# Kernel tuning notes

Measured on AMD Instinct MI355X. Metric: run time of the kernel, lower is better.

Reference implementation:

```python
import jax, jax.numpy as jnp
import numpy as np

N = 50000      # nodes
E = 800000     # edges (avg degree 16)
D_IN = 128     # node_feature_dim
H = 256        # hidden_dim
EPS = 1e-5     # BatchNorm eps


def setup_inputs() -> dict:
    key = jax.random.key(0)
    ks = jax.random.split(key, 32)
    inp = {
        "x": jax.random.normal(ks[0], (N, D_IN), jnp.float32),
        "edge_index": jax.random.randint(ks[1], (2, E), 0, N, jnp.int32),
    }
    dims = [(D_IN, H), (H, H), (H, H)]
    k = 2
    for i, (din, dout) in enumerate(dims):
        s = 1.0 / np.sqrt(din)
        inp[f"Wl{i}"] = jax.random.uniform(ks[k], (din, dout), jnp.float32, -s, s); k += 1
        inp[f"bl{i}"] = jax.random.uniform(ks[k], (dout,), jnp.float32, -s, s); k += 1
        inp[f"Wr{i}"] = jax.random.uniform(ks[k], (din, dout), jnp.float32, -s, s); k += 1
        inp[f"g{i}"] = jnp.ones((dout,), jnp.float32)
        inp[f"b{i}"] = jnp.zeros((dout,), jnp.float32)
        inp[f"rm{i}"] = jax.random.normal(ks[k], (dout,), jnp.float32) * 0.1; k += 1
        inp[f"rv{i}"] = jax.random.uniform(ks[k], (dout,), jnp.float32, 0.5, 1.5); k += 1
    return inp


def _sage(x, src, dst, Wl, bl, Wr):
    # PyG SAGEConv (aggr='mean'): out = lin_l(mean_{j in N(i)} x_j) + lin_r(x_i)
    deg = jax.ops.segment_sum(jnp.ones((src.shape[0],), x.dtype), dst, num_segments=N)
    agg = jax.ops.segment_sum(x[src], dst, num_segments=N)  # [N, d_in]
    mean = agg / jnp.maximum(deg, 1.0)[:, None]
    return mean @ Wl + bl + x @ Wr


def _bn(x, g, b, rm, rv):
    # eval-mode BatchNorm1d with running stats
    return (x - rm) * (g * jax.lax.rsqrt(rv + EPS)) + b


def reference(x, edge_index,
              Wl0, bl0, Wr0, g0, b0, rm0, rv0,
              Wl1, bl1, Wr1, g1, b1, rm1, rv1,
              Wl2, bl2, Wr2, g2, b2, rm2, rv2):
    src, dst = edge_index[0], edge_index[1]
    h = jax.nn.relu(_bn(_sage(x, src, dst, Wl0, bl0, Wr0), g0, b0, rm0, rv0))
    h = jax.nn.relu(_bn(_sage(h, src, dst, Wl1, bl1, Wr1), g1, b1, rm1, rv1))
    h = _bn(_sage(h, src, dst, Wl2, bl2, Wr2), g2, b2, rm2, rv2)
    return h  # [N, H] node embeddings (dropout is identity in eval mode)
```

## Files before the change

kernel.cpp:

```cpp
#include <hip/hip_runtime.h>
#include <hip/hip_bf16.h>

#define NNODES 50000
#define NEDGES 800000
#define HID 256
#define BN_EPS 1e-5f
#define SCAN_B ((NNODES + 255) / 256)

typedef __attribute__((ext_vector_type(8))) short short8v;
typedef __attribute__((ext_vector_type(4))) float f32x4;
typedef __attribute__((ext_vector_type(2))) float f32x2;

__device__ inline void load_lds16(const void* g, void* l) {
    __builtin_amdgcn_global_load_lds(
        (const __attribute__((address_space(1))) unsigned int*)g,
        (__attribute__((address_space(3))) unsigned int*)l, 16, 0, 0);
}

__global__ void k_countrank(const int* __restrict__ ei, int* __restrict__ cnt,
                            int* __restrict__ rank, int nE) {
    int e = blockIdx.x * blockDim.x + threadIdx.x;
    if (e < nE) rank[e] = atomicAdd(&cnt[ei[nE + e]], 1);
}

__global__ void k_bsum(const int* __restrict__ cnt, int* __restrict__ loc,
                       int* __restrict__ bsum, int n) {
    __shared__ int sh[256];
    int tid = threadIdx.x;
    int i = blockIdx.x * 256 + tid;
    int v = (i < n) ? cnt[i] : 0;
    sh[tid] = v;
    __syncthreads();
    for (int off = 1; off < 256; off <<= 1) {
        int t = (tid >= off) ? sh[tid - off] : 0;
        __syncthreads();
        sh[tid] += t;
        __syncthreads();
    }
    if (i < n) loc[i] = sh[tid] - v;
    if (tid == 255) bsum[blockIdx.x] = sh[255];
}

__global__ void k_bscan(int* __restrict__ bsum, int nb) {
    __shared__ int sh[256];
    int tid = threadIdx.x;
    int v = (tid < nb) ? bsum[tid] : 0;
    sh[tid] = v;
    __syncthreads();
    for (int off = 1; off < 256; off <<= 1) {
        int t = (tid >= off) ? sh[tid - off] : 0;
        __syncthreads();
        sh[tid] += t;
        __syncthreads();
    }
    if (tid < nb) bsum[tid] = sh[tid] - v;
}

__global__ void k_addoff(const int* __restrict__ loc, const int* __restrict__ bsum,
                         int* __restrict__ rowptr, int n, int nE) {
    int i = blockIdx.x * 256 + threadIdx.x;
    if (i < n) rowptr[i] = loc[i] + bsum[blockIdx.x];
    if (i == 0) rowptr[n] = nE;
}

__global__ void k_fill2(const int* __restrict__ ei, const int* __restrict__ rowptr,
                        const int* __restrict__ rank, int* __restrict__ col, int nE) {
    int e = blockIdx.x * blockDim.x + threadIdx.x;
    if (e < nE) col[rowptr[ei[nE + e]] + rank[e]] = ei[e];
}

#define PREP_CAST 1600000
#define PREP_TR   327680
__global__ void k_prep(const float* __restrict__ x,
                       __hip_bfloat16* __restrict__ xb, unsigned char* __restrict__ x8,
                       const float* __restrict__ s0, const float* __restrict__ s1,
                       const float* __restrict__ s2, const float* __restrict__ s3,
                       const float* __restrict__ s4, const float* __restrict__ s5,
                       __hip_bfloat16* __restrict__ d0, __hip_bfloat16* __restrict__ d1,
                       __hip_bfloat16* __restrict__ d2, __hip_bfloat16* __restrict__ d3,
                       __hip_bfloat16* __restrict__ d4, __hip_bfloat16* __restrict__ d5,
                       int* __restrict__ cnt) {
    int f = blockIdx.x * blockDim.x + threadIdx.x;
    if (f < PREP_CAST) {
        float4 v = *(const float4*)(x + f * 4);
        union { uint2 u; unsigned short s[4]; } ob;
        ob.s[0] = __bfloat16_as_ushort(__float2bfloat16(v.x));
        ob.s[1] = __bfloat16_as_ushort(__float2bfloat16(v.y));
        ob.s[2] = __bfloat16_as_ushort(__float2bfloat16(v.z));
        ob.s[3] = __bfloat16_as_ushort(__float2bfloat16(v.w));
        *(uint2*)(xb + f * 4) = ob.u;
        int p = __builtin_amdgcn_cvt_pk_fp8_f32(v.x, v.y, 0, false);
        p = __builtin_amdgcn_cvt_pk_fp8_f32(v.z, v.w, p, true);
        *(int*)(x8 + f * 4) = p;
    } else if (f < PREP_CAST + PREP_TR) {
        int r = f - PREP_CAST;
        const float* src; __hip_bfloat16* dst; int K; int i;
        if (r < 65536) {
            K = 128;
            if (r < 32768) { src = s0; dst = d0; i = r; }
            else           { src = s1; dst = d1; i = r - 32768; }
        } else {
            K = 256;
            int q = r - 65536;
            int wsel = q >> 16;
            i = q & 65535;
            src = (wsel == 0) ? s2 : (wsel == 1) ? s3 : (wsel == 2) ? s4 : s5;
            dst = (wsel == 0) ? d2 : (wsel == 1) ? d3 : (wsel == 2) ? d4 : d5;
        }
        int k = i >> 8;
        int nn = i & 255;
        dst[nn * K + k] = __float2bfloat16(src[i]);
    } else {
        int i = f - PREP_CAST - PREP_TR;
        if (i < NNODES) cnt[i] = 0;
    }
}

template <int D, int U>
__global__ void k_meanf8(const unsigned char* __restrict__ x8,
                         const int* __restrict__ rowptr, const int* __restrict__ col,
                         __hip_bfloat16* __restrict__ mean, int n) {
    constexpr int CPL = D / 16;
    constexpr int R = 64 / CPL;
    int gw = (blockIdx.x * blockDim.x + threadIdx.x) >> 6;
    int lane = threadIdx.x & 63;
    if (gw >= n) return;
    int beg = rowptr[gw], end = rowptr[gw + 1];
    int sub = lane / CPL;
    int fpos = lane % CPL;
    const uint4* base = (const uint4*)x8;

    float acc[16];
#pragma unroll
    for (int j = 0; j < 16; j++) acc[j] = 0.f;

    for (int p0 = beg; p0 < end; p0 += U * R) {
        int idx[U]; bool ok[U];
#pragma unroll
        for (int u = 0; u < U; u++) {
            int p = p0 + u * R + sub;
            ok[u] = (p < end);
            idx[u] = ok[u] ? col[p] : 0;
        }
        uint4 v[U];
#pragma unroll
        for (int u = 0; u < U; u++) {
            uint4 t = {0u, 0u, 0u, 0u};
            if (ok[u]) t = base[(size_t)idx[u] * CPL + fpos];
            v[u] = t;
        }
#pragma unroll
        for (int u = 0; u < U; u++) {
            const unsigned int uu[4] = {v[u].x, v[u].y, v[u].z, v[u].w};
#pragma unroll
            for (int q = 0; q < 4; q++) {
                f32x2 lo = __builtin_amdgcn_cvt_pk_f32_fp8(uu[q], false);
                f32x2 hi = __builtin_amdgcn_cvt_pk_f32_fp8(uu[q], true);
                acc[4 * q + 0] += lo.x;
                acc[4 * q + 1] += lo.y;
                acc[4 * q + 2] += hi.x;
                acc[4 * q + 3] += hi.y;
            }
        }
    }

    if constexpr (R >= 8) {
#pragma unroll
        for (int j = 0; j < 16; j++) acc[j] += __shfl_xor(acc[j], 8, 64);
    }
#pragma unroll
    for (int j = 0; j < 16; j++) acc[j] += __shfl_xor(acc[j], 16, 64);
#pragma unroll
    for (int j = 0; j < 16; j++) acc[j] += __shfl_xor(acc[j], 32, 64);

    if (sub == 0) {
        float inv = (end > beg) ? 1.f / (float)(end - beg) : 0.f;
        union { uint4 v[2]; unsigned short s[16]; } o;
#pragma unroll
        for (int j = 0; j < 16; j++)
            o.s[j] = __bfloat16_as_ushort(__float2bfloat16(acc[j] * inv));
        uint4* dst = (uint4*)(mean + (size_t)gw * D + fpos * 16);
        dst[0] = o.v[0];
        dst[1] = o.v[1];
    }
}

template <int KH, typename OutT, int RELU, int W8>
__launch_bounds__(256, 2)
__global__ void k_gemm3(const __hip_bfloat16* __restrict__ A1,
                        const __hip_bfloat16* __restrict__ A2,
                        const __hip_bfloat16* __restrict__ W1t,
                        const __hip_bfloat16* __restrict__ W2t,
                        const float* __restrict__ bl,
                        const float* __restrict__ g,
                        const float* __restrict__ bb,
                        const float* __restrict__ rm,
                        const float* __restrict__ rv,
                        OutT* __restrict__ out, unsigned char* __restrict__ out8,
                        int n) {
    constexpr int NSTEP = KH / 16;
    constexpr int K8TOT = KH / 4;
    __shared__ uint4 ldsv[4096];
    char* lds = (char*)ldsv;
    int tid = threadIdx.x;
    int l = (blockIdx.x & 7) * (gridDim.x >> 3) + (blockIdx.x >> 3);
    int rb = l >> 2, ct = l & 3;
    int colbase = ct * 64;

#pragma unroll
    for (int it = 0; it < K8TOT / 4; it++) {
        int j = tid + it * 256;
        int k8 = j >> 6, c = j & 63;
        const __hip_bfloat16* src =
            (k8 < KH / 8) ? (W1t + (size_t)(colbase + c) * KH + k8 * 8)
                          : (W2t + (size_t)(colbase + c) * KH + (k8 - KH / 8) * 8);
        load_lds16(src, lds + (size_t)j * 16);
    }

    int lane = tid & 63, wv = tid >> 6;
    int quad = lane >> 4, ml = lane & 15;
    int row0 = rb * 256 + wv * 64;

    const short8v* p1[4];
    const short8v* p2[4];
#pragma unroll
    for (int i = 0; i < 4; i++) {
        int r = row0 + i * 16 + ml;
        if (r > n - 1) r = n - 1;
        p1[i] = (const short8v*)(A1 + (size_t)r * KH) + quad;
        p2[i] = (const short8v*)(A2 + (size_t)r * KH) + quad;
    }

    f32x4 acc[4][4];
#pragma unroll
    for (int i = 0; i < 4; i++)
#pragma unroll
        for (int t = 0; t < 4; t++) acc[i][t] = {0.f, 0.f, 0.f, 0.f};

    short8v ab[4][4];
#pragma unroll
    for (int s = 0; s < 3; s++) {
        const short8v* const* pp = (s < NSTEP / 2) ? p1 : p2;
        int sh = (s < NSTEP / 2) ? s : s - NSTEP / 2;
#pragma unroll
        for (int i = 0; i < 4; i++) ab[s][i] = pp[i][sh * 4];
    }
    __syncthreads();

#pragma unroll
    for (int s = 0; s < NSTEP; s++) {
        int sn = s + 3;
        if (sn < NSTEP) {
            const short8v* const* pp = (sn < NSTEP / 2) ? p1 : p2;
            int sh = (sn < NSTEP / 2) ? sn : sn - NSTEP / 2;
#pragma unroll
            for (int i = 0; i < 4; i++) ab[sn & 3][i] = pp[i][sh * 4];
        }
        short8v bfr[4];
#pragma unroll
        for (int t = 0; t < 4; t++)
            bfr[t] = *(const short8v*)(lds + ((size_t)((s * 4 + quad) * 64 + t * 16 + ml)) * 16);
#pragma unroll
        for (int t = 0; t < 4; t++)
#pragma unroll
            for (int i = 0; i < 4; i++)
                acc[i][t] = __builtin_amdgcn_mfma_f32_16x16x32_bf16(
                    ab[s & 3][i], bfr[t], acc[i][t], 0, 0, 0);
    }

    __syncthreads();
    float* scr = (float*)(lds + wv * 16384);
#pragma unroll
    for (int t = 0; t < 4; t++) {
        int c = colbase + t * 16 + ml;
        float sv = g[c] * rsqrtf(rv[c] + BN_EPS);
        float tv = (bl[c] - rm[c]) * sv + bb[c];
#pragma unroll
        for (int i = 0; i < 4; i++)
#pragma unroll
            for (int r = 0; r < 4; r++) {
                float v = acc[i][t][r] * sv + tv;
                if (RELU) v = fmaxf(v, 0.f);
                scr[(i * 16 + quad * 4 + r) * 64 + t * 16 + ml] = v;
            }
    }
    int rl8 = lane >> 3, c8 = (lane & 7) * 8;
#pragma unroll
    for (int p = 0; p < 8; p++) {
        int rowl = p * 8 + rl8;
        int row = row0 + rowl;
        f32x4 v0 = *(const f32x4*)(scr + rowl * 64 + c8);
        f32x4 v1 = *(const f32x4*)(scr + rowl * 64 + c8 + 4);
        if (row < n) {
            if constexpr (sizeof(OutT) == 2) {
                union { uint4 u; unsigned short s[8]; } o;
                o.s[0] = __bfloat16_as_ushort(__float2bfloat16(v0.x));
                o.s[1] = __bfloat16_as_ushort(__float2bfloat16(v0.y));
                o.s[2] = __bfloat16_as_ushort(__float2bfloat16(v0.z));
                o.s[3] = __bfloat16_as_ushort(__float2bfloat16(v0.w));
                o.s[4] = __bfloat16_as_ushort(__float2bfloat16(v1.x));
                o.s[5] = __bfloat16_as_ushort(__float2bfloat16(v1.y));
                o.s[6] = __bfloat16_as_ushort(__float2bfloat16(v1.z));
                o.s[7] = __bfloat16_as_ushort(__float2bfloat16(v1.w));
                *(uint4*)(out + (size_t)row * HID + colbase + c8) = o.u;
            } else {
                float* dst = (float*)out + (size_t)row * HID + colbase + c8;
                *(f32x4*)dst = v0;
                *(f32x4*)(dst + 4) = v1;
            }
            if constexpr (W8) {
                int lo = __builtin_amdgcn_cvt_pk_fp8_f32(v0.x, v0.y, 0, false);
                lo = __builtin_amdgcn_cvt_pk_fp8_f32(v0.z, v0.w, lo, true);
                int hi = __builtin_amdgcn_cvt_pk_fp8_f32(v1.x, v1.y, 0, false);
                hi = __builtin_amdgcn_cvt_pk_fp8_f32(v1.z, v1.w, hi, true);
                uint2 u2 = {(unsigned)lo, (unsigned)hi};
                *(uint2*)(out8 + (size_t)row * HID + colbase + c8) = u2;
            }
        }
    }
}

extern "C" void kernel_launch(void* const* d_in, const int* in_sizes, int n_in,
                              void* d_out, int out_size, void* d_ws, size_t ws_size,
                              hipStream_t stream) {
    const float* x = (const float*)d_in[0];
    const int* ei = (const int*)d_in[1];
    const float *Wl[3], *blv[3], *Wr[3], *g[3], *bb[3], *rm[3], *rv[3];
    for (int i = 0; i < 3; i++) {
        int b = 2 + i * 7;
        Wl[i]  = (const float*)d_in[b + 0];
        blv[i] = (const float*)d_in[b + 1];
        Wr[i]  = (const float*)d_in[b + 2];
        g[i]   = (const float*)d_in[b + 3];
        bb[i]  = (const float*)d_in[b + 4];
        rm[i]  = (const float*)d_in[b + 5];
        rv[i]  = (const float*)d_in[b + 6];
    }

    char* ob = (char*)d_out;
    __hip_bfloat16* xb = (__hip_bfloat16*)ob;
    __hip_bfloat16* h0 = (__hip_bfloat16*)(ob + (size_t)NNODES * 128 * 2);

    char* w = (char*)d_ws;
    size_t off = 0;
    auto alloc = [&](size_t bytes) {
        void* p = w + off;
        off += (bytes + 255) & ~(size_t)255;
        return p;
    };
    int* rowptr = (int*)alloc((NNODES + 1) * sizeof(int));
    int* cnt    = (int*)alloc(NNODES * sizeof(int));
    int* loc    = (int*)alloc(NNODES * sizeof(int));
    int* bsum   = (int*)alloc(SCAN_B * sizeof(int));
    int* rank   = (int*)alloc(NEDGES * sizeof(int));
    int* col    = (int*)alloc(NEDGES * sizeof(int));
    __hip_bfloat16* meanb = (__hip_bfloat16*)alloc((size_t)NNODES * HID * 2);
    __hip_bfloat16* h1    = (__hip_bfloat16*)alloc((size_t)NNODES * HID * 2);
    unsigned char* x8   = (unsigned char*)alloc((size_t)NNODES * 128);
    unsigned char* h0f8 = (unsigned char*)alloc((size_t)NNODES * HID);
    unsigned char* h1f8 = (unsigned char*)alloc((size_t)NNODES * HID);
    __hip_bfloat16* Wt[6];
    int Ks[6] = {128, 128, 256, 256, 256, 256};
    for (int i = 0; i < 6; i++) Wt[i] = (__hip_bfloat16*)alloc((size_t)Ks[i] * HID * 2);

    int prepTotal = PREP_CAST + PREP_TR + NNODES;
    k_prep<<<(prepTotal + 255) / 256, 256, 0, stream>>>(
        x, xb, x8, Wl[0], Wr[0], Wl[1], Wr[1], Wl[2], Wr[2],
        Wt[0], Wt[1], Wt[2], Wt[3], Wt[4], Wt[5], cnt);

    k_countrank<<<(NEDGES + 255) / 256, 256, 0, stream>>>(ei, cnt, rank, NEDGES);
    k_bsum<<<SCAN_B, 256, 0, stream>>>(cnt, loc, bsum, NNODES);
    k_bscan<<<1, 256, 0, stream>>>(bsum, SCAN_B);
    k_addoff<<<SCAN_B, 256, 0, stream>>>(loc, bsum, rowptr, NNODES, NEDGES);
    k_fill2<<<(NEDGES + 255) / 256, 256, 0, stream>>>(ei, rowptr, rank, col, NEDGES);

    int meanBlocks = (NNODES * 64 + 255) / 256;
    int gemmBlocks = ((NNODES + 255) / 256) * 4;

    k_meanf8<128, 2><<<meanBlocks, 256, 0, stream>>>(x8, rowptr, col, meanb, NNODES);
    k_gemm3<128, __hip_bfloat16, 1, 1><<<gemmBlocks, 256, 0, stream>>>(meanb, xb, Wt[0], Wt[1],
        blv[0], g[0], bb[0], rm[0], rv[0], h0, h0f8, NNODES);

    k_meanf8<256, 4><<<meanBlocks, 256, 0, stream>>>(h0f8, rowptr, col, meanb, NNODES);
    k_gemm3<256, __hip_bfloat16, 1, 1><<<gemmBlocks, 256, 0, stream>>>(meanb, h0, Wt[2], Wt[3],
        blv[1], g[1], bb[1], rm[1], rv[1], h1, h1f8, NNODES);

    k_meanf8<256, 4><<<meanBlocks, 256, 0, stream>>>(h1f8, rowptr, col, meanb, NNODES);
    k_gemm3<256, float, 0, 0><<<gemmBlocks, 256, 0, stream>>>(meanb, h1, Wt[4], Wt[5],
        blv[2], g[2], bb[2], rm[2], rv[2], (float*)d_out, (unsigned char*)nullptr, NNODES);
}
```

Baseline: 397.4 us.

## Use 512-thread GEMM blocks with smaller per-wave tiles and XOR-swizzled LDS

The fused SAGE GEMM now runs 8 waves per block, each computing 32 rows instead of 64. This halves the accumulator and A-fragment registers per wave, raising occupancy and latency hiding. The weight tile in LDS and the epilogue scratch buffer are XOR-swizzled to reduce bank conflicts on B-fragment reads and on the transposed output stores. Each block must still fit LDS for both the weights and the per-wave scratch, and there are fewer MFMAs per loaded B fragment, so B reuse drops.

After: 404.4 us. Within noise of the previous version (+1.8%).

```diff
diff --git a/kernel.cpp b/kernel.cpp
--- a/kernel.cpp
+++ b/kernel.cpp
@@ -186,8 +186,8 @@
 }
 
 template <int KH, typename OutT, int RELU, int W8>
-__launch_bounds__(256, 2)
-__global__ void k_gemm3(const __hip_bfloat16* __restrict__ A1,
+__launch_bounds__(512, 4)
+__global__ void k_gemm4(const __hip_bfloat16* __restrict__ A1,
                         const __hip_bfloat16* __restrict__ A2,
                         const __hip_bfloat16* __restrict__ W1t,
                         const __hip_bfloat16* __restrict__ W2t,
@@ -199,7 +199,7 @@
                         OutT* __restrict__ out, unsigned char* __restrict__ out8,
                         int n) {
     constexpr int NSTEP = KH / 16;
-    constexpr int K8TOT = KH / 4;
+    constexpr int NCH = 16 * KH;
     __shared__ uint4 ldsv[4096];
     char* lds = (char*)ldsv;
     int tid = threadIdx.x;
@@ -208,42 +208,43 @@
     int colbase = ct * 64;
 
 #pragma unroll
-    for (int it = 0; it < K8TOT / 4; it++) {
-        int j = tid + it * 256;
+    for (int it = 0; it < NCH / 512; it++) {
+        int j = tid + it * 512;
         int k8 = j >> 6, c = j & 63;
+        int cs = c ^ (k8 & 7);
         const __hip_bfloat16* src =
-            (k8 < KH / 8) ? (W1t + (size_t)(colbase + c) * KH + k8 * 8)
-                          : (W2t + (size_t)(colbase + c) * KH + (k8 - KH / 8) * 8);
+            (k8 < KH / 8) ? (W1t + (size_t)(colbase + cs) * KH + k8 * 8)
+                          : (W2t + (size_t)(colbase + cs) * KH + (k8 - KH / 8) * 8);
         load_lds16(src, lds + (size_t)j * 16);
     }
 
     int lane = tid & 63, wv = tid >> 6;
     int quad = lane >> 4, ml = lane & 15;
-    int row0 = rb * 256 + wv * 64;
-
-    const short8v* p1[4];
-    const short8v* p2[4];
-#pragma unroll
-    for (int i = 0; i < 4; i++) {
+    int row0 = rb * 256 + wv * 32;
+
+    const short8v* p1[2];
+    const short8v* p2[2];
+#pragma unroll
+    for (int i = 0; i < 2; i++) {
         int r = row0 + i * 16 + ml;
         if (r > n - 1) r = n - 1;
         p1[i] = (const short8v*)(A1 + (size_t)r * KH) + quad;
         p2[i] = (const short8v*)(A2 + (size_t)r * KH) + quad;
     }
 
-    f32x4 acc[4][4];
-#pragma unroll
-    for (int i = 0; i < 4; i++)
+    f32x4 acc[2][4];
+#pragma unroll
+    for (int i = 0; i < 2; i++)
 #pragma unroll
         for (int t = 0; t < 4; t++) acc[i][t] = {0.f, 0.f, 0.f, 0.f};
 
-    short8v ab[4][4];
+    short8v ab[4][2];
 #pragma unroll
     for (int s = 0; s < 3; s++) {
         const short8v* const* pp = (s < NSTEP / 2) ? p1 : p2;
         int sh = (s < NSTEP / 2) ? s : s - NSTEP / 2;
 #pragma unroll
-        for (int i = 0; i < 4; i++) ab[s][i] = pp[i][sh * 4];
+        for (int i = 0; i < 2; i++) ab[s][i] = pp[i][sh * 4];
     }
     __syncthreads();
 
@@ -254,43 +255,46 @@
             const short8v* const* pp = (sn < NSTEP / 2) ? p1 : p2;
             int sh = (sn < NSTEP / 2) ? sn : sn - NSTEP / 2;
 #pragma unroll
-            for (int i = 0; i < 4; i++) ab[sn & 3][i] = pp[i][sh * 4];
-        }
-        short8v bfr[4];
-#pragma unroll
-        for (int t = 0; t < 4; t++)
-            bfr[t] = *(const short8v*)(lds + ((size_t)((s * 4 + quad) * 64 + t * 16 + ml)) * 16);
-#pragma unroll
-        for (int t = 0; t < 4; t++)
-#pragma unroll
-            for (int i = 0; i < 4; i++)
-                acc[i][t] = __builtin_amdgcn_mfma_f32_16x16x32_bf16(
-                    ab[s & 3][i], bfr[t], acc[i][t], 0, 0, 0);
+            for (int i = 0; i < 2; i++) ab[sn & 3][i] = pp[i][sh * 4];
+        }
+        int k8 = s * 4 + quad;
+#pragma unroll
+        for (int t = 0; t < 4; t++) {
+            short8v bfr = *(const short8v*)(
+                lds + (size_t)((k8 * 64 + ((t * 16 + ml) ^ (k8 & 7))) * 16));
+            acc[0][t] = __builtin_amdgcn_mfma_f32_16x16x32_bf16(
+                ab[s & 3][0], bfr, acc[0][t], 0, 0, 0);
+            acc[1][t] = __builtin_amdgcn_mfma_f32_16x16x32_bf16(
+                ab[s & 3][1], bfr, acc[1][t], 0, 0, 0);
+        }
     }
 
     __syncthreads();
-    float* scr = (float*)(lds + wv * 16384);
+    char* scrb = lds + wv * 8192;
 #pragma unroll
     for (int t = 0; t < 4; t++) {
         int c = colbase + t * 16 + ml;
         float sv = g[c] * rsqrtf(rv[c] + BN_EPS);
         float tv = (bl[c] - rm[c]) * sv + bb[c];
 #pragma unroll
-        for (int i = 0; i < 4; i++)
+        for (int i = 0; i < 2; i++)
 #pragma unroll
             for (int r = 0; r < 4; r++) {
                 float v = acc[i][t][r] * sv + tv;
                 if (RELU) v = fmaxf(v, 0.f);
-                scr[(i * 16 + quad * 4 + r) * 64 + t * 16 + ml] = v;
+                int row = i * 16 + quad * 4 + r;
+                int off = row * 256 + (((t * 16 + ml) * 4) ^ ((row & 7) << 4));
+                *(float*)(scrb + off) = v;
             }
     }
     int rl8 = lane >> 3, c8 = (lane & 7) * 8;
 #pragma unroll
-    for (int p = 0; p < 8; p++) {
+    for (int p = 0; p < 4; p++) {
         int rowl = p * 8 + rl8;
         int row = row0 + rowl;
-        f32x4 v0 = *(const f32x4*)(scr + rowl * 64 + c8);
-        f32x4 v1 = *(const f32x4*)(scr + rowl * 64 + c8 + 4);
+        int sw = (rowl & 7) << 4;
+        f32x4 v0 = *(const f32x4*)(scrb + rowl * 256 + ((c8 * 4) ^ sw));
+        f32x4 v1 = *(const f32x4*)(scrb + rowl * 256 + ((c8 * 4 + 16) ^ sw));
         if (row < n) {
             if constexpr (sizeof(OutT) == 2) {
                 union { uint4 u; unsigned short s[8]; } o;
@@ -378,14 +382,14 @@
     int gemmBlocks = ((NNODES + 255) / 256) * 4;
 
     k_meanf8<128, 2><<<meanBlocks, 256, 0, stream>>>(x8, rowptr, col, meanb, NNODES);
-    k_gemm3<128, __hip_bfloat16, 1, 1><<<gemmBlocks, 256, 0, stream>>>(meanb, xb, Wt[0], Wt[1],
+    k_gemm4<128, __hip_bfloat16, 1, 1><<<gemmBlocks, 512, 0, stream>>>(meanb, xb, Wt[0], Wt[1],
         blv[0], g[0], bb[0], rm[0], rv[0], h0, h0f8, NNODES);
 
     k_meanf8<256, 4><<<meanBlocks, 256, 0, stream>>>(h0f8, rowptr, col, meanb, NNODES);
-    k_gemm3<256, __hip_bfloat16, 1, 1><<<gemmBlocks, 256, 0, stream>>>(meanb, h0, Wt[2], Wt[3],
+    k_gemm4<256, __hip_bfloat16, 1, 1><<<gemmBlocks, 512, 0, stream>>>(meanb, h0, Wt[2], Wt[3],
         blv[1], g[1], bb[1], rm[1], rv[1], h1, h1f8, NNODES);
 
     k_meanf8<256, 4><<<meanBlocks, 256, 0, stream>>>(h1f8, rowptr, col, meanb, NNODES);
-    k_gemm3<256, float, 0, 0><<<gemmBlocks, 256, 0, stream>>>(meanb, h1, Wt[4], Wt[5],
+    k_gemm4<256, float, 0, 0><<<gemmBlocks, 512, 0, stream>>>(meanb, h1, Wt[4], Wt[5],
         blv[2], g[2], bb[2], rm[2], rv[2], (float*)d_out, (unsigned char*)nullptr, NNODES);
 }
```
